# Kernel tuning notes

Measured on AMD Instinct MI355X. Metric: run time of the kernel, lower is better.

Reference implementation:

```python
import jax, jax.numpy as jnp
import numpy as np

B, H, P, D, NF = 4, 8, 196, 64, 8


def setup_inputs() -> dict:
    key = jax.random.key(0)
    ks = jax.random.split(key, 10)
    grid = (jnp.arange(NF * 5, dtype=jnp.float32) + 1.0).reshape(5, NF)
    inv = 1.0 / np.sqrt(D)
    return {
        "q": jax.random.normal(ks[0], (B, H, P, D), jnp.float32),
        "k": jax.random.normal(ks[1], (B, H, P, D), jnp.float32),
        "scale": jnp.ones((1,), jnp.float32),  # accepted but unused (as in original)
        "grid": grid,
        "grid_outer": grid,
        "base_weight": jax.random.uniform(ks[2], (D, D), jnp.float32),
        "coef_q": jax.random.uniform(ks[3], (D, NF, 5), jnp.float32),
        "coef_k": jax.random.uniform(ks[4], (D, NF, 5), jnp.float32),
        "coef_qk": jax.random.uniform(ks[5], (P * P, NF, 5), jnp.float32),
        "scale_base": jnp.ones((1, H, 5, P, D), jnp.float32),
        "scale_sp": jnp.ones((1, H, 5, P, D), jnp.float32),
        "coef_qk_outer": jnp.ones((1, 1, 5, P, P), jnp.float32),
        "lin_q_w": jax.random.uniform(ks[6], (5 * D, D), jnp.float32, -inv, inv),
        "lin_q_b": jax.random.uniform(ks[7], (5 * D,), jnp.float32, -inv, inv),
        "lin_k_w": jax.random.uniform(ks[8], (5 * D, D), jnp.float32, -inv, inv),
        "lin_k_b": jax.random.uniform(ks[9], (5 * D,), jnp.float32, -inv, inv),
    }


def reference(q, k, scale, grid, grid_outer, base_weight, coef_q, coef_k, coef_qk,
              scale_base, scale_sp, coef_qk_outer, lin_q_w, lin_q_b, lin_k_w, lin_k_b):
    b, h, p, d = q.shape
    nf = grid.shape[1]
    qf = q.reshape(-1, d)
    kf = k.reshape(-1, d)
    # lin_q / lin_k -> [B*H*P, 5, D]
    q5 = (qf @ lin_q_w.T + lin_q_b).reshape(-1, 5, d)
    k5 = (kf @ lin_k_w.T + lin_k_b).reshape(-1, 5, d)
    # base path (note: reshape [BHP,5,D] -> [B,H,5,P,D] is a raw row-major remap, as in torch)
    base_q = (jax.nn.silu(q5) @ base_weight.T).reshape(b, h, 5, p, d)
    base_k = (jax.nn.silu(k5) @ base_weight.T).reshape(b, h, 5, p, d)
    # inner sin-basis expansion: sin(grid * x) weighted by coef, summed over num_f
    cq = jnp.transpose(coef_q, (2, 1, 0))  # [5, nf, d]
    ck = jnp.transpose(coef_k, (2, 1, 0))
    sin_q = jnp.sin(grid[None, :, :, None] * q5[:, :, None, :])  # [BHP,5,nf,d]
    f_q = (sin_q * cq[None]).reshape(b, h, 5, nf, p, d).sum(3)   # [B,H,5,P,D]
    sin_k = jnp.sin(grid[None, :, :, None] * k5[:, :, None, :])
    f_k = (sin_k * ck[None]).reshape(b, h, 5, nf, p, d).sum(3)
    f_q = f_q * scale_sp + base_q * scale_base
    f_k = f_k * scale_sp + base_k * scale_base
    # sum_d(sigmoid(q)_d + sigmoid(k)_d) == sum_d sig(q) + sum_d sig(k): outer add of reductions
    aq = jax.nn.sigmoid(f_q).sum(-1)  # [B,H,5,P]
    ak = jax.nn.sigmoid(f_k).sum(-1)
    qk = (aq[..., :, None] + ak[..., None, :]).reshape(b * h, 5, p * p)
    # outer sin-basis expansion over the P*P score map
    cqk = jnp.transpose(coef_qk, (2, 1, 0))  # [5, nf, P*P]
    sin_qk = jnp.sin(grid_outer[None, :, :, None] * qk[:, :, None, :])  # [BH,5,nf,PP]
    f = (sin_qk * cqk[None]).reshape(b, h, 5, nf, p, p).sum(3)  # [B,H,5,P,P]
    f = (f * coef_qk_outer).sum(2)  # [B,H,P,P]
    return jax.nn.softmax(f, axis=-1)
```

## Files before the change

### kernel.cpp

```cpp
#include <hip/hip_runtime.h>
#include <math.h>

#define BHP 6272

static __device__ __forceinline__ unsigned short f2bf(float x) {
  unsigned u = __float_as_uint(x);
  unsigned r = (u + 0x7fffu + ((u >> 16) & 1u)) >> 16;
  return (unsigned short)r;
}

__global__ __launch_bounds__(256) void k0_fuse_pack(
    const float* __restrict__ cqk, const float* __restrict__ cqo,
    unsigned short* __restrict__ F16,
    const float* __restrict__ Wq, const float* __restrict__ Wk,
    const float* __restrict__ BW, float4* __restrict__ Wq4,
    float4* __restrict__ Wk4, float4* __restrict__ BW4)
{
  __shared__ float ld[196 * 41];
  const int t = threadIdx.x;
  if (blockIdx.x >= 196) {
    const int e = (blockIdx.x - 196) * 256 + t;
    if (e < 5120) {
      const int o = e % 320, c4 = e / 320;
      Wq4[e] = *reinterpret_cast<const float4*>(Wq + o * 64 + c4 * 4);
    } else if (e < 10240) {
      const int e2 = e - 5120;
      const int o = e2 % 320, c4 = e2 / 320;
      Wk4[e2] = *reinterpret_cast<const float4*>(Wk + o * 64 + c4 * 4);
    } else if (e < 11264) {
      const int e2 = e - 10240;
      const int d = e2 % 64, c4 = e2 / 64;
      BW4[e2] = *reinterpret_cast<const float4*>(BW + d * 64 + c4 * 4);
    }
    return;
  }
  const int i = blockIdx.x;
  const float4* src = reinterpret_cast<const float4*>(cqk + (size_t)i * 7840);
  for (int e4 = t; e4 < 1960; e4 += 256) {
    const float4 v = src[e4];
    const int flat = e4 * 4;
    const int j = flat / 40, m0 = flat % 40;
    float* dst = &ld[j * 41 + m0];
    dst[0] = v.x; dst[1] = v.y; dst[2] = v.z; dst[3] = v.w;
  }
  __syncthreads();
  for (int e = t; e < 7840; e += 256) {
    const int mq = e / 196, j = e % 196;
    const int s = mq >> 3, f = mq & 7;
    const float val = ld[j * 41 + f * 5 + s];
    F16[(size_t)i * 7840 + e] = f2bf(val * cqo[(s * 196 + i) * 196 + j]);
  }
}

__global__ __launch_bounds__(320) void k1_lin_base(
    const float* __restrict__ qx, const float* __restrict__ kx,
    const float4* __restrict__ Wq4, const float* __restrict__ bq_,
    const float4* __restrict__ Wk4, const float* __restrict__ bk_,
    const float4* __restrict__ BW4,
    float* __restrict__ y5q, float* __restrict__ y5k,
    float* __restrict__ baseq, float* __restrict__ basek)
{
  const bool kside = blockIdx.x >= 392;
  const float* x = kside ? kx : qx;
  const float4* W4 = kside ? Wk4 : Wq4;
  const float* bias = kside ? bk_ : bq_;
  float* y5 = kside ? y5k : y5q;
  float* basef = kside ? basek : baseq;
  const int r0 = (kside ? blockIdx.x - 392 : blockIdx.x) * 16;

  __shared__ float xs[16][64];
  __shared__ float sy[16][320];
  const int t = threadIdx.x;
  const int rh = t / 160;
  const int ct = t % 160;
  const int oA = 2 * ct, oB = oA + 1;
  const int rbase = rh * 8;

  for (int idx = t; idx < 16 * 64; idx += 320)
    xs[idx >> 6][idx & 63] = x[(size_t)(r0 + (idx >> 6)) * 64 + (idx & 63)];
  __syncthreads();

  {
    float accA[8], accB[8];
#pragma unroll
    for (int rr = 0; rr < 8; ++rr) { accA[rr] = 0.f; accB[rr] = 0.f; }
#pragma unroll
    for (int g = 0; g < 4; ++g) {
      float4 wA[4], wB[4];
#pragma unroll
      for (int u = 0; u < 4; ++u) {
        wA[u] = W4[(g * 4 + u) * 320 + oA];
        wB[u] = W4[(g * 4 + u) * 320 + oB];
      }
#pragma unroll
      for (int u = 0; u < 4; ++u) {
#pragma unroll
        for (int rr = 0; rr < 8; ++rr) {
          const float4 x4 =
              *reinterpret_cast<const float4*>(&xs[rbase + rr][(g * 4 + u) * 4]);
          accA[rr] = fmaf(x4.x, wA[u].x, accA[rr]);
          accB[rr] = fmaf(x4.x, wB[u].x, accB[rr]);
          accA[rr] = fmaf(x4.y, wA[u].y, accA[rr]);
          accB[rr] = fmaf(x4.y, wB[u].y, accB[rr]);
          accA[rr] = fmaf(x4.z, wA[u].z, accA[rr]);
          accB[rr] = fmaf(x4.z, wB[u].z, accB[rr]);
          accA[rr] = fmaf(x4.w, wA[u].w, accA[rr]);
          accB[rr] = fmaf(x4.w, wB[u].w, accB[rr]);
        }
      }
    }
    const float bbA = bias[oA], bbB = bias[oB];
#pragma unroll
    for (int rr = 0; rr < 8; ++rr) {
      const float yA = accA[rr] + bbA;
      const float yB = accB[rr] + bbB;
      *reinterpret_cast<float2*>(&y5[(size_t)(r0 + rbase + rr) * 320 + oA]) =
          make_float2(yA, yB);
      sy[rbase + rr][oA] = yA / (1.f + __expf(-yA));
      sy[rbase + rr][oB] = yB / (1.f + __expf(-yB));
    }
  }
  __syncthreads();
  {
    const int s = oA >> 6;
    const int dA = oA & 63, dB = dA + 1;
    float accA[8], accB[8];
#pragma unroll
    for (int rr = 0; rr < 8; ++rr) { accA[rr] = 0.f; accB[rr] = 0.f; }
#pragma unroll
    for (int g = 0; g < 4; ++g) {
      float4 wA[4], wB[4];
#pragma unroll
      for (int u = 0; u < 4; ++u) {
        wA[u] = BW4[(g * 4 + u) * 64 + dA];
        wB[u] = BW4[(g * 4 + u) * 64 + dB];
      }
#pragma unroll
      for (int u = 0; u < 4; ++u) {
#pragma unroll
        for (int rr = 0; rr < 8; ++rr) {
          const float4 x4 = *reinterpret_cast<const float4*>(
              &sy[rbase + rr][s * 64 + (g * 4 + u) * 4]);
          accA[rr] = fmaf(x4.x, wA[u].x, accA[rr]);
          accB[rr] = fmaf(x4.x, wB[u].x, accB[rr]);
          accA[rr] = fmaf(x4.y, wA[u].y, accA[rr]);
          accB[rr] = fmaf(x4.y, wB[u].y, accB[rr]);
          accA[rr] = fmaf(x4.z, wA[u].z, accA[rr]);
          accB[rr] = fmaf(x4.z, wB[u].z, accB[rr]);
          accA[rr] = fmaf(x4.w, wA[u].w, accA[rr]);
          accB[rr] = fmaf(x4.w, wB[u].w, accB[rr]);
        }
      }
    }
#pragma unroll
    for (int rr = 0; rr < 8; ++rr)
      *reinterpret_cast<float2*>(&basef[(size_t)(r0 + rbase + rr) * 320 + oA]) =
          make_float2(accA[rr], accB[rr]);
  }
}

__global__ __launch_bounds__(1024) void k2_act(
    const float* __restrict__ y5q, const float* __restrict__ bq,
    const float* __restrict__ y5k, const float* __restrict__ bk,
    const float* __restrict__ gridI, const float* __restrict__ gridO,
    const float* __restrict__ cq, const float* __restrict__ ck,
    const float* __restrict__ ssp, const float* __restrict__ sbase,
    float2* __restrict__ tq, float2* __restrict__ tk)
{
  __shared__ float cl[40][65];
  __shared__ float gli[40], glo[40];
  const int t = threadIdx.x;
  const int wave = t >> 6, lane = t & 63;
  const int gi = blockIdx.x * 16 + wave;
  const bool kside = gi >= 31360;
  const int idx = kside ? gi - 31360 : gi;

  {
    const float* coef = kside ? ck : cq;
    for (int e = t; e < 2560; e += 1024) {
      const int d = e / 40, r = e % 40;
      const int f = r / 5, s = r % 5;
      cl[s * 8 + f][d] = coef[e];
    }
    if (t < 40) { gli[t] = gridI[t]; glo[t] = gridO[t]; }
  }
  __syncthreads();

  const int p2 = idx % 196;
  const int s2 = (idx / 196) % 5;
  const int bh = idx / 980;
  const int h = bh & 7;
  const int d = lane;
  const int i0 = s2 * 196 + p2;
  const float* y5 = kside ? y5k : y5q;
  const float* basef = kside ? bk : bq;
  const float basev =
      basef[(size_t)(bh * 196 + i0 / 5) * 320 + (i0 % 5) * 64 + d];

  const int j0 = s2 * 1568 + p2;
  int p = j0 / 40;
  int m = j0 % 40;
  const float* y5b = y5 + (size_t)bh * 196 * 320 + d;
  float fv = 0.f;
#pragma unroll
  for (int f2 = 0; f2 < 8; ++f2) {
    const float g = gli[m];
    const float qv = y5b[p * 320 + (m >> 3) * 64];
    fv = fmaf(__sinf(g * qv), cl[m][d], fv);
    p += 4; m += 36;
    if (m >= 40) { m -= 40; p += 1; }
  }
  const int so = ((h * 5 + s2) * 196 + p2) * 64 + d;
  const float v = fv * ssp[so] + basev * sbase[so];
  float sg = 1.f / (1.f + __expf(-v));
#pragma unroll
  for (int off = 32; off > 0; off >>= 1) sg += __shfl_xor(sg, off);
  if (lane < 8) {
    const int mm = s2 * 8 + lane;
    const float g = rintf(glo[mm]);
    const float n0 = rintf(sg * 0.15915494309f);
    float r = fmaf(n0, -6.28318548f, sg);
    r = fmaf(n0, 1.74845553e-7f, r);
    const float u = g * r;
    float2* tab = kside ? tk : tq;
    tab[bh * 7840 + mm * 196 + p2] = make_float2(__sinf(u), __cosf(u));
  }
}

__global__ __launch_bounds__(256, 6) void k3_outer(
    const float2* __restrict__ tq, const float2* __restrict__ tk,
    const unsigned short* __restrict__ F16, float* __restrict__ out)
{
  const int t = threadIdx.x;
  const int wave = t >> 6, lane = t & 63;
  const int bid = blockIdx.x;
  const int swz = (bid & 7) * 196 + (bid >> 3);
  const int i = swz >> 3;
  const int bhg = swz & 7;
  const int bh = bhg * 4 + wave;
  __shared__ unsigned short fs[7840];
  __shared__ float2 sqs[4][40];

  {
    const float4* Fp = reinterpret_cast<const float4*>(F16 + (size_t)i * 7840);
    float4* fs4 = reinterpret_cast<float4*>(fs);
    for (int e = t; e < 980; e += 256) fs4[e] = Fp[e];
    if (lane < 40) sqs[wave][lane] = tq[(size_t)bh * 7840 + lane * 196 + i];
  }
  __syncthreads();

  const bool hasb = lane < 34;
  const int ja = 2 * lane;
  const int jb = hasb ? (128 + 2 * lane) : (2 * lane);
  const float2* tk0 = tk + (size_t)bh * 7840;

  float a0x = 0.f, a0y = 0.f, a1x = 0.f, a1y = 0.f;
#pragma unroll 4
  for (int mm = 0; mm < 40; ++mm) {
    const int o = mm * 196;
    const unsigned ua = *reinterpret_cast<const unsigned*>(&fs[o + ja]);
    const unsigned ub = *reinterpret_cast<const unsigned*>(&fs[o + jb]);
    const float fax = __uint_as_float(ua << 16);
    const float fay = __uint_as_float(ua & 0xffff0000u);
    const float fbx = __uint_as_float(ub << 16);
    const float fby = __uint_as_float(ub & 0xffff0000u);
    const float2 s0 = sqs[wave][mm];
    const float4 k0a = *reinterpret_cast<const float4*>(&tk0[o + ja]);
    const float4 k0b = *reinterpret_cast<const float4*>(&tk0[o + jb]);
    a0x = fmaf(fmaf(s0.x, k0a.y, s0.y * k0a.x), fax, a0x);
    a0y = fmaf(fmaf(s0.x, k0a.w, s0.y * k0a.z), fay, a0y);
    a1x = fmaf(fmaf(s0.x, k0b.y, s0.y * k0b.x), fbx, a1x);
    a1y = fmaf(fmaf(s0.x, k0b.w, s0.y * k0b.z), fby, a1y);
  }

  const float mB = hasb ? fmaxf(a1x, a1y) : -INFINITY;
  float mx = fmaxf(fmaxf(a0x, a0y), mB);
#pragma unroll
  for (int off = 32; off > 0; off >>= 1) mx = fmaxf(mx, __shfl_xor(mx, off));
  const float e0 = __expf(a0x - mx);
  const float e1 = __expf(a0y - mx);
  const float e2 = hasb ? __expf(a1x - mx) : 0.f;
  const float e3 = hasb ? __expf(a1y - mx) : 0.f;
  float ss = e0 + e1 + e2 + e3;
#pragma unroll
  for (int off = 32; off > 0; off >>= 1) ss += __shfl_xor(ss, off);
  const float inv = 1.f / ss;
  float2* op = reinterpret_cast<float2*>(out + (size_t)(bh * 196 + i) * 196);
  op[lane] = make_float2(e0 * inv, e1 * inv);
  if (hasb) op[64 + lane] = make_float2(e2 * inv, e3 * inv);
}

extern "C" void kernel_launch(void* const* d_in, const int* in_sizes, int n_in,
                              void* d_out, int out_size, void* d_ws, size_t ws_size,
                              hipStream_t stream) {
  const float* q          = (const float*)d_in[0];
  const float* k          = (const float*)d_in[1];
  const float* grid       = (const float*)d_in[3];
  const float* grid_outer = (const float*)d_in[4];
  const float* base_w     = (const float*)d_in[5];
  const float* coef_q     = (const float*)d_in[6];
  const float* coef_k     = (const float*)d_in[7];
  const float* coef_qk    = (const float*)d_in[8];
  const float* scale_base = (const float*)d_in[9];
  const float* scale_sp   = (const float*)d_in[10];
  const float* cqo        = (const float*)d_in[11];
  const float* lqw        = (const float*)d_in[12];
  const float* lqb        = (const float*)d_in[13];
  const float* lkw        = (const float*)d_in[14];
  const float* lkb        = (const float*)d_in[15];
  float* out = (float*)d_out;

  const size_t SLAB = (size_t)BHP * 320;
  float* q5 = (float*)d_ws;
  float* k5 = q5 + SLAB;
  float* bq = k5 + SLAB;
  float* bk = bq + SLAB;
  unsigned short* F16 = (unsigned short*)(bk + SLAB);
  float2* tabq = (float2*)(F16 + 1536640);
  float2* tabk = tabq + 250880;
  float* wpack = (float*)(tabk + 250880);
  float4* Wq4 = (float4*)wpack;
  float4* Wk4 = Wq4 + 5120;
  float4* BW4 = Wk4 + 5120;

  k0_fuse_pack<<<dim3(240), dim3(256), 0, stream>>>(
      coef_qk, cqo, F16, lqw, lkw, base_w, Wq4, Wk4, BW4);
  k1_lin_base<<<dim3(784), dim3(320), 0, stream>>>(
      q, k, Wq4, lqb, Wk4, lkb, BW4, q5, k5, bq, bk);
  k2_act<<<dim3(62720 / 16), dim3(1024), 0, stream>>>(
      q5, bq, k5, bk, grid, grid_outer, coef_q, coef_k,
      scale_sp, scale_base, tabq, tabk);
  k3_outer<<<dim3(1568), dim3(256), 0, stream>>>(tabq, tabk, F16, out);
}
```

Before: 96.60 us.

## Store key-side sin/cos table as packed bf16 and widen per-lane column tiles

The key-side sin/cos table written by the activation kernel is now packed as two bf16 values per 32-bit word instead of a float2, which halves the bytes the outer-product kernel reads per column. The outer kernel is also remapped so each of 49 active lanes handles four consecutive columns. It issues one 128-bit table load, one 64-bit shared load and one float4 output store per lane, replacing the earlier two-by-two split with a partial second half. The cost is reduced precision in the key-side trig values that feed the softmax logits, and 15 idle lanes per wave.

Result: faster. 90.68 us (-6.1%).

```diff
diff --git a/kernel.cpp b/kernel.cpp
--- a/kernel.cpp
+++ b/kernel.cpp
@@ -165,7 +165,7 @@
     const float* __restrict__ gridI, const float* __restrict__ gridO,
     const float* __restrict__ cq, const float* __restrict__ ck,
     const float* __restrict__ ssp, const float* __restrict__ sbase,
-    float2* __restrict__ tq, float2* __restrict__ tk)
+    float2* __restrict__ tq, unsigned* __restrict__ tk16)
 {
   __shared__ float cl[40][65];
   __shared__ float gli[40], glo[40];
@@ -222,13 +222,17 @@
     float r = fmaf(n0, -6.28318548f, sg);
     r = fmaf(n0, 1.74845553e-7f, r);
     const float u = g * r;
-    float2* tab = kside ? tk : tq;
-    tab[bh * 7840 + mm * 196 + p2] = make_float2(__sinf(u), __cosf(u));
+    const float sv_ = __sinf(u), cv_ = __cosf(u);
+    const int ti = bh * 7840 + mm * 196 + p2;
+    if (kside)
+      tk16[ti] = ((unsigned)f2bf(cv_) << 16) | (unsigned)f2bf(sv_);
+    else
+      tq[ti] = make_float2(sv_, cv_);
   }
 }
 
 __global__ __launch_bounds__(256, 6) void k3_outer(
-    const float2* __restrict__ tq, const float2* __restrict__ tk,
+    const float2* __restrict__ tq, const unsigned* __restrict__ tk16,
     const unsigned short* __restrict__ F16, float* __restrict__ out)
 {
   const int t = threadIdx.x;
@@ -249,45 +253,50 @@
   }
   __syncthreads();
 
-  const bool hasb = lane < 34;
-  const int ja = 2 * lane;
-  const int jb = hasb ? (128 + 2 * lane) : (2 * lane);
-  const float2* tk0 = tk + (size_t)bh * 7840;
-
-  float a0x = 0.f, a0y = 0.f, a1x = 0.f, a1y = 0.f;
+  const bool act = lane < 49;
+  const int j0 = act ? 4 * lane : 192;
+  const unsigned* tkb = tk16 + (size_t)bh * 7840 + j0;
+
+  float a0 = 0.f, a1 = 0.f, a2 = 0.f, a3 = 0.f;
 #pragma unroll 4
   for (int mm = 0; mm < 40; ++mm) {
     const int o = mm * 196;
-    const unsigned ua = *reinterpret_cast<const unsigned*>(&fs[o + ja]);
-    const unsigned ub = *reinterpret_cast<const unsigned*>(&fs[o + jb]);
-    const float fax = __uint_as_float(ua << 16);
-    const float fay = __uint_as_float(ua & 0xffff0000u);
-    const float fbx = __uint_as_float(ub << 16);
-    const float fby = __uint_as_float(ub & 0xffff0000u);
+    const uint4 kp = *reinterpret_cast<const uint4*>(tkb + o);
+    const uint2 fp = *reinterpret_cast<const uint2*>(&fs[o + j0]);
     const float2 s0 = sqs[wave][mm];
-    const float4 k0a = *reinterpret_cast<const float4*>(&tk0[o + ja]);
-    const float4 k0b = *reinterpret_cast<const float4*>(&tk0[o + jb]);
-    a0x = fmaf(fmaf(s0.x, k0a.y, s0.y * k0a.x), fax, a0x);
-    a0y = fmaf(fmaf(s0.x, k0a.w, s0.y * k0a.z), fay, a0y);
-    a1x = fmaf(fmaf(s0.x, k0b.y, s0.y * k0b.x), fbx, a1x);
-    a1y = fmaf(fmaf(s0.x, k0b.w, s0.y * k0b.z), fby, a1y);
-  }
-
-  const float mB = hasb ? fmaxf(a1x, a1y) : -INFINITY;
-  float mx = fmaxf(fmaxf(a0x, a0y), mB);
+    const float sn0 = __uint_as_float(kp.x << 16);
+    const float cs0 = __uint_as_float(kp.x & 0xffff0000u);
+    const float sn1 = __uint_as_float(kp.y << 16);
+    const float cs1 = __uint_as_float(kp.y & 0xffff0000u);
+    const float sn2 = __uint_as_float(kp.z << 16);
+    const float cs2 = __uint_as_float(kp.z & 0xffff0000u);
+    const float sn3 = __uint_as_float(kp.w << 16);
+    const float cs3 = __uint_as_float(kp.w & 0xffff0000u);
+    const float f0 = __uint_as_float(fp.x << 16);
+    const float f1 = __uint_as_float(fp.x & 0xffff0000u);
+    const float f2 = __uint_as_float(fp.y << 16);
+    const float f3 = __uint_as_float(fp.y & 0xffff0000u);
+    a0 = fmaf(fmaf(s0.x, cs0, s0.y * sn0), f0, a0);
+    a1 = fmaf(fmaf(s0.x, cs1, s0.y * sn1), f1, a1);
+    a2 = fmaf(fmaf(s0.x, cs2, s0.y * sn2), f2, a2);
+    a3 = fmaf(fmaf(s0.x, cs3, s0.y * sn3), f3, a3);
+  }
+
+  float mx = act ? fmaxf(fmaxf(a0, a1), fmaxf(a2, a3)) : -INFINITY;
 #pragma unroll
   for (int off = 32; off > 0; off >>= 1) mx = fmaxf(mx, __shfl_xor(mx, off));
-  const float e0 = __expf(a0x - mx);
-  const float e1 = __expf(a0y - mx);
-  const float e2 = hasb ? __expf(a1x - mx) : 0.f;
-  const float e3 = hasb ? __expf(a1y - mx) : 0.f;
+  const float e0 = act ? __expf(a0 - mx) : 0.f;
+  const float e1 = act ? __expf(a1 - mx) : 0.f;
+  const float e2 = act ? __expf(a2 - mx) : 0.f;
+  const float e3 = act ? __expf(a3 - mx) : 0.f;
   float ss = e0 + e1 + e2 + e3;
 #pragma unroll
   for (int off = 32; off > 0; off >>= 1) ss += __shfl_xor(ss, off);
   const float inv = 1.f / ss;
-  float2* op = reinterpret_cast<float2*>(out + (size_t)(bh * 196 + i) * 196);
-  op[lane] = make_float2(e0 * inv, e1 * inv);
-  if (hasb) op[64 + lane] = make_float2(e2 * inv, e3 * inv);
+  if (act) {
+    float4* op = reinterpret_cast<float4*>(out + (size_t)(bh * 196 + i) * 196 + j0);
+    *op = make_float4(e0 * inv, e1 * inv, e2 * inv, e3 * inv);
+  }
 }
 
 extern "C" void kernel_launch(void* const* d_in, const int* in_sizes, int n_in,
@@ -317,7 +326,7 @@
   float* bk = bq + SLAB;
   unsigned short* F16 = (unsigned short*)(bk + SLAB);
   float2* tabq = (float2*)(F16 + 1536640);
-  float2* tabk = tabq + 250880;
+  unsigned* tabk = (unsigned*)(tabq + 250880);
   float* wpack = (float*)(tabk + 250880);
   float4* Wq4 = (float4*)wpack;
   float4* Wk4 = Wq4 + 5120;
```
